# Optimization experiments

Measured on AMD Instinct MI355X. Metric: run time of the kernel, lower is better.

## Reference

```python
import jax, jax.numpy as jnp
import numpy as np

HIDDEN = 1024
HEADS = 16
K = 8
B = 4
S = 2048
LN_EPS = 1e-5


def setup_inputs() -> dict:
    key = jax.random.key(0)
    ks = jax.random.split(key, 16)
    E = HIDDEN
    w = lambda kk, shape: jax.random.normal(kk, shape, dtype=jnp.float32) * 0.02
    return {
        "representations": jax.random.normal(ks[0], (B, S, E), dtype=jnp.float32),
        "attention_mask": jnp.zeros((B, S), dtype=jnp.float32),
        "queries": jax.random.normal(ks[1], (K, E), dtype=jnp.float32),
        "Wq": w(ks[2], (K, E, E)), "bq": jnp.zeros((K, E), jnp.float32),
        "Wk": w(ks[3], (K, E, E)), "bk": jnp.zeros((K, E), jnp.float32),
        "Wv": w(ks[4], (K, E, E)), "bv": jnp.zeros((K, E), jnp.float32),
        "Wo": w(ks[5], (K, E, E)), "bo": jnp.zeros((K, E), jnp.float32),
        "Wp": w(ks[6], (K, E, E)), "bp": jnp.zeros((K, E), jnp.float32),
        "gamma": jnp.ones((E,), jnp.float32),
        "beta": jnp.zeros((E,), jnp.float32),
    }


def reference(representations, attention_mask, queries, Wq, bq, Wk, bk, Wv, bv,
              Wo, bo, Wp, bp, gamma, beta):
    k, E = queries.shape
    Bq, Sq, _ = representations.shape
    H = HEADS
    Dh = E // H
    # per-k query projection (query length is 1)
    q = jnp.einsum('ke,kfe->kf', queries, Wq) + bq          # (k, E)
    q = q.reshape(k, H, Dh) * (Dh ** -0.5)                  # (k, H, Dh)
    # stacked key/value projections across all k attention layers
    Kp = jnp.einsum('bse,kfe->kbsf', representations, Wk) + bk[:, None, None, :]
    Vp = jnp.einsum('bse,kfe->kbsf', representations, Wv) + bv[:, None, None, :]
    Kp = Kp.reshape(k, Bq, Sq, H, Dh)
    Vp = Vp.reshape(k, Bq, Sq, H, Dh)
    # single-query attention scores, additive float mask per batch over keys
    scores = jnp.einsum('khd,kbshd->kbhs', q, Kp)           # (k, B, H, S)
    scores = scores + attention_mask[None, :, None, :]
    probs = jax.nn.softmax(scores, axis=-1)
    ctx = jnp.einsum('kbhs,kbshd->kbhd', probs, Vp).reshape(k, Bq, E)
    # MHA out_proj, then per-k output projection
    attn_out = jnp.einsum('kbe,kfe->kbf', ctx, Wo) + bo[:, None, :]
    out = jnp.einsum('kbe,kfe->kbf', attn_out, Wp) + bp[:, None, :]
    # concat along query-slot dim -> (B, k, E), then LayerNorm over E
    out = out.transpose(1, 0, 2)
    mu = out.mean(-1, keepdims=True)
    var = ((out - mu) ** 2).mean(-1, keepdims=True)
    return gamma * (out - mu) * jax.lax.rsqrt(var + LN_EPS) + beta
```

## Files before the change

### kernel.cpp

```cpp
#include <hip/hip_runtime.h>
#include <hip/hip_bf16.h>
#include <stdint.h>

#define E_  1024
#define H_  16
#define D_  64
#define K_  8
#define B_  4
#define S_  2048
#define KH_ 128

typedef __attribute__((ext_vector_type(8))) short   short8;
typedef __attribute__((ext_vector_type(8))) ushort  ushort8;
typedef __attribute__((ext_vector_type(4))) ushort  ushort4v;
typedef __attribute__((ext_vector_type(4))) float   f32x4;

__device__ __forceinline__ ushort f2bf(float x){
  union { float f; uint32_t u; } v; v.f = x;
  return (ushort)((v.u + 0x7FFFu + ((v.u >> 16) & 1u)) >> 16);
}

__device__ __forceinline__ void lds_barrier(){
  asm volatile("s_waitcnt lgkmcnt(0)" ::: "memory");
  __builtin_amdgcn_s_barrier();
}

__global__ __launch_bounds__(256) void k1_qs(const float* __restrict__ queries,
                                             const float* __restrict__ Wq,
                                             const float* __restrict__ bq,
                                             float* __restrict__ qs){
  int gw = (blockIdx.x * 256 + threadIdx.x) >> 6;
  int lane = threadIdx.x & 63;
  int k = gw >> 10, f = gw & 1023;
  const float* wrow = Wq + ((size_t)(k*E_) + f)*E_;
  const float* qrow = queries + k*E_;
  float acc = 0.f;
  #pragma unroll
  for (int j = 0; j < 4; j++){
    int e = (j*64 + lane)*4;
    float4 w = *(const float4*)(wrow + e);
    float4 q = *(const float4*)(qrow + e);
    acc += w.x*q.x + w.y*q.y + w.z*q.z + w.w*q.w;
  }
  #pragma unroll
  for (int off = 32; off; off >>= 1) acc += __shfl_down(acc, off);
  if (lane == 0) qs[k*E_ + f] = (acc + bq[k*E_ + f]) * 0.125f;
}

__global__ __launch_bounds__(256) void k2_qk(const float* __restrict__ qs,
                                             const float* __restrict__ Wk,
                                             const float* __restrict__ bk,
                                             ushort* __restrict__ qkb,
                                             float* __restrict__ qb){
  int bid = blockIdx.x;
  int eq = bid & 3;
  int kh = bid >> 2;
  int k = kh >> 4, h = kh & 15;
  __shared__ float qsh[64];
  int t = threadIdx.x;
  if (t < 64) qsh[t] = qs[k*E_ + h*64 + t];
  __syncthreads();
  int e = eq*256 + t;
  const float* wbase = Wk + ((size_t)(k*E_) + h*64)*E_ + e;
  float a = 0.f;
  #pragma unroll 8
  for (int d = 0; d < 64; d++) a += qsh[d] * wbase[(size_t)d*E_];
  qkb[kh*E_ + e] = f2bf(a);
  if (eq == 0 && t == 0){
    float s = 0.f;
    for (int d = 0; d < 64; d++) s += qsh[d] * bk[k*E_ + h*64 + d];
    qb[kh] = s;
  }
}

__global__ __launch_bounds__(256) void k3_scores(const float* __restrict__ rep,
                                                 const ushort* __restrict__ qkb,
                                                 float* __restrict__ scoresP){
  __shared__ __align__(16) ushort As[2][64][40];
  __shared__ __align__(16) ushort Bs[2][128][40];
  int bid = blockIdx.x;
  int ks = bid & 3, m = (bid >> 2) & 31, b = bid >> 7;
  int t = threadIdx.x, wv = t >> 6, lane = t & 63;
  int l0 = lane & 15, l1 = lane >> 4;
  int wr = wv >> 1, wc = wv & 1;
  int arow = t >> 2, acg = t & 3;
  int brow = t >> 1, bhalf = t & 1;
  const float*  aSrc = rep + ((size_t)(b*S_) + m*64 + arow)*E_ + ks*256 + acg*4;
  const ushort* bSrc = qkb + (size_t)brow*E_ + ks*256 + bhalf*16;

  f32x4 acc[2][4];
  #pragma unroll
  for (int mt = 0; mt < 2; mt++)
    #pragma unroll
    for (int nt = 0; nt < 4; nt++) acc[mt][nt] = (f32x4){0.f,0.f,0.f,0.f};

  float4  va[2][2];
  ushort8 vb[2][2];
  #pragma unroll
  for (int p = 0; p < 2; p++){
    va[p][0] = *(const float4*)(aSrc + p*32);
    va[p][1] = *(const float4*)(aSrc + p*32 + 16);
    vb[p][0] = *(const ushort8*)(bSrc + p*32);
    vb[p][1] = *(const ushort8*)(bSrc + p*32 + 8);
  }
  #pragma unroll
  for (int j = 0; j < 2; j++){
    ushort4v u;
    u[0]=f2bf(va[0][j].x); u[1]=f2bf(va[0][j].y); u[2]=f2bf(va[0][j].z); u[3]=f2bf(va[0][j].w);
    *(ushort4v*)&As[0][arow][acg*4 + j*16] = u;
    *(ushort8*)&Bs[0][brow][bhalf*16 + j*8] = vb[0][j];
  }
  lds_barrier();

  #pragma unroll
  for (int c = 0; c < 8; c++){
    const int cur = c & 1;
    short8 af[2], bf[4];
    #pragma unroll
    for (int mt = 0; mt < 2; mt++)
      af[mt] = *(const short8*)&As[cur][wr*32 + mt*16 + l0][l1*8];
    #pragma unroll
    for (int nt = 0; nt < 4; nt++)
      bf[nt] = *(const short8*)&Bs[cur][wc*64 + nt*16 + l0][l1*8];
    #pragma unroll
    for (int mt = 0; mt < 2; mt++)
      #pragma unroll
      for (int nt = 0; nt < 4; nt++)
        acc[mt][nt] = __builtin_amdgcn_mfma_f32_16x16x32_bf16(af[mt], bf[nt], acc[mt][nt], 0,0,0);
    if (c < 6){
      const int p = c & 1;
      va[p][0] = *(const float4*)(aSrc + (c+2)*32);
      va[p][1] = *(const float4*)(aSrc + (c+2)*32 + 16);
      vb[p][0] = *(const ushort8*)(bSrc + (c+2)*32);
      vb[p][1] = *(const ushort8*)(bSrc + (c+2)*32 + 8);
    }
    if (c < 7){
      const int p = (c+1) & 1;
      #pragma unroll
      for (int j = 0; j < 2; j++){
        ushort4v u;
        u[0]=f2bf(va[p][j].x); u[1]=f2bf(va[p][j].y); u[2]=f2bf(va[p][j].z); u[3]=f2bf(va[p][j].w);
        *(ushort4v*)&As[p][arow][acg*4 + j*16] = u;
        *(ushort8*)&Bs[p][brow][bhalf*16 + j*8] = vb[p][j];
      }
    }
    lds_barrier();
  }
  float* obase = scoresP + (size_t)ks*((size_t)B_*KH_*S_) + (size_t)(b*KH_)*S_;
  #pragma unroll
  for (int mt = 0; mt < 2; mt++){
    #pragma unroll
    for (int nt = 0; nt < 4; nt++){
      int kh = wc*64 + nt*16 + l0;
      int s  = m*64 + wr*32 + mt*16 + l1*4;
      float* op = obase + (size_t)kh*S_ + s;
      #pragma unroll
      for (int r = 0; r < 4; r++) op[r] = acc[mt][nt][r];
    }
  }
}

__global__ __launch_bounds__(256) void k4_softmax(const float* __restrict__ scoresP,
                                                  const float* __restrict__ qb,
                                                  const float* __restrict__ mask,
                                                  ushort* __restrict__ probs,
                                                  float* __restrict__ wrep){
  __shared__ float red[4];
  const size_t P = (size_t)B_*KH_*S_;
  int row = blockIdx.x;
  int b = row >> 7, kh = row & 127;
  int t = threadIdx.x, wv = t >> 6, lane = t & 63;
  {
    float4 z = {0.f, 0.f, 0.f, 0.f};
    *(float4*)(wrep + ((size_t)blockIdx.x*1024 + t*4)) = z;
  }
  const float* x = scoresP + (size_t)row * S_ + t*8;
  const float* mrow = mask + b*S_ + t*8;
  float qbv = qb[kh];
  float v[8];
  #pragma unroll
  for (int h = 0; h < 2; h++){
    float4 p0 = *(const float4*)(x + h*4);
    float4 p1 = *(const float4*)(x + h*4 + P);
    float4 p2 = *(const float4*)(x + h*4 + 2*P);
    float4 p3 = *(const float4*)(x + h*4 + 3*P);
    float4 mm = *(const float4*)(mrow + h*4);
    v[h*4+0] = (p0.x + p1.x) + (p2.x + p3.x) + qbv + mm.x;
    v[h*4+1] = (p0.y + p1.y) + (p2.y + p3.y) + qbv + mm.y;
    v[h*4+2] = (p0.z + p1.z) + (p2.z + p3.z) + qbv + mm.z;
    v[h*4+3] = (p0.w + p1.w) + (p2.w + p3.w) + qbv + mm.w;
  }
  float m = v[0];
  #pragma unroll
  for (int i = 1; i < 8; i++) m = fmaxf(m, v[i]);
  #pragma unroll
  for (int off = 32; off; off >>= 1) m = fmaxf(m, __shfl_down(m, off));
  if (lane == 0) red[wv] = m;
  __syncthreads();
  float M = fmaxf(fmaxf(red[0], red[1]), fmaxf(red[2], red[3]));
  __syncthreads();
  float s = 0.f;
  #pragma unroll
  for (int i = 0; i < 8; i++){ v[i] = __expf(v[i] - M); s += v[i]; }
  #pragma unroll
  for (int off = 32; off; off >>= 1) s += __shfl_down(s, off);
  if (lane == 0) red[wv] = s;
  __syncthreads();
  float inv = 1.0f / (red[0] + red[1] + red[2] + red[3]);
  ushort8 o;
  #pragma unroll
  for (int i = 0; i < 8; i++) o[i] = f2bf(v[i] * inv);
  *(ushort8*)(probs + (size_t)row*S_ + t*8) = o;
}

__global__ __launch_bounds__(256) void k5_wrep(const ushort* __restrict__ probs,
                                               const float* __restrict__ rep,
                                               float* __restrict__ wrep){
  __shared__ __align__(16) ushort As[2][128][40];
  __shared__ __align__(16) ushort Bs[2][64][40];
  int bid = blockIdx.x;
  int et = bid & 15, b = (bid >> 4) & 3, sp = bid >> 6;
  int t = threadIdx.x, wv = t >> 6, lane = t & 63;
  int l0 = lane & 15, l1 = lane >> 4;
  int wr = wv >> 1, wc = wv & 1;
  int arow = t >> 1, ahalf = t & 1;
  int bsrow = t >> 3, beg = t & 7;
  const ushort* aSrc = probs + (size_t)(b*KH_ + arow)*S_ + sp*256 + ahalf*16;
  const float*  bSrc = rep + ((size_t)(b*S_) + sp*256 + bsrow)*E_ + et*64 + beg*8;

  f32x4 acc[4][2];
  #pragma unroll
  for (int mt = 0; mt < 4; mt++)
    #pragma unroll
    for (int nt = 0; nt < 2; nt++) acc[mt][nt] = (f32x4){0.f,0.f,0.f,0.f};

  ushort8 va[2][2];
  float4  vb[2][2];
  #pragma unroll
  for (int p = 0; p < 2; p++){
    va[p][0] = *(const ushort8*)(aSrc + p*32);
    va[p][1] = *(const ushort8*)(aSrc + p*32 + 8);
    vb[p][0] = *(const float4*)(bSrc + (size_t)(p*32)*E_);
    vb[p][1] = *(const float4*)(bSrc + (size_t)(p*32)*E_ + 4);
  }
  {
    *(ushort8*)&As[0][arow][ahalf*16]     = va[0][0];
    *(ushort8*)&As[0][arow][ahalf*16 + 8] = va[0][1];
    int rot = (beg & 3) * 8;
    int sw = (bsrow + rot) & 31;
    #pragma unroll
    for (int j = 0; j < 2; j++){
      float vv[4] = {vb[0][j].x, vb[0][j].y, vb[0][j].z, vb[0][j].w};
      #pragma unroll
      for (int jj = 0; jj < 4; jj++)
        Bs[0][beg*8 + j*4 + jj][sw] = f2bf(vv[jj]);
    }
  }
  lds_barrier();

  #pragma unroll
  for (int c = 0; c < 8; c++){
    const int cur = c & 1;
    short8 af[4], bf[2];
    #pragma unroll
    for (int mt = 0; mt < 4; mt++)
      af[mt] = *(const short8*)&As[cur][wr*64 + mt*16 + l0][l1*8];
    #pragma unroll
    for (int nt = 0; nt < 2; nt++){
      int e_loc = wc*32 + nt*16 + l0;
      int sstart = (l1*8 + ((e_loc >> 3) & 3)*8) & 31;
      bf[nt] = *(const short8*)&Bs[cur][e_loc][sstart];
    }
    #pragma unroll
    for (int mt = 0; mt < 4; mt++)
      #pragma unroll
      for (int nt = 0; nt < 2; nt++)
        acc[mt][nt] = __builtin_amdgcn_mfma_f32_16x16x32_bf16(af[mt], bf[nt], acc[mt][nt], 0,0,0);
    if (c < 6){
      const int p = c & 1;
      va[p][0] = *(const ushort8*)(aSrc + (c+2)*32);
      va[p][1] = *(const ushort8*)(aSrc + (c+2)*32 + 8);
      vb[p][0] = *(const float4*)(bSrc + (size_t)((c+2)*32)*E_);
      vb[p][1] = *(const float4*)(bSrc + (size_t)((c+2)*32)*E_ + 4);
    }
    if (c < 7){
      const int p = (c+1) & 1;
      *(ushort8*)&As[p][arow][ahalf*16]     = va[p][0];
      *(ushort8*)&As[p][arow][ahalf*16 + 8] = va[p][1];
      int rot = (beg & 3) * 8;
      int sw = (bsrow + rot) & 31;
      #pragma unroll
      for (int j = 0; j < 2; j++){
        float vv[4] = {vb[p][j].x, vb[p][j].y, vb[p][j].z, vb[p][j].w};
        #pragma unroll
        for (int jj = 0; jj < 4; jj++)
          Bs[p][beg*8 + j*4 + jj][sw] = f2bf(vv[jj]);
      }
    }
    lds_barrier();
  }
  float* obase = wrep + (size_t)(b*KH_)*E_ + et*64;
  #pragma unroll
  for (int mt = 0; mt < 4; mt++){
    #pragma unroll
    for (int nt = 0; nt < 2; nt++){
      int kh = wr*64 + mt*16 + l1*4;
      int e  = wc*32 + nt*16 + l0;
      #pragma unroll
      for (int r = 0; r < 4; r++)
        unsafeAtomicAdd(&obase[(size_t)(kh + r)*E_ + e], acc[mt][nt][r]);
    }
  }
}

__global__ __launch_bounds__(256) void k6_ctx(const float* __restrict__ wrep,
                                              const float* __restrict__ Wv,
                                              const float* __restrict__ bv,
                                              float* __restrict__ ctx){
  int gw = (blockIdx.x*256 + threadIdx.x) >> 6;
  int lane = threadIdx.x & 63;
  int k = gw >> 10, f = gw & 1023;
  int h = f >> 6;
  const float* wrow = Wv + ((size_t)(k*E_) + f)*E_;
  const float* x0 = wrep + ((size_t)(0*KH_) + k*16 + h)*E_;
  const float* x1 = wrep + ((size_t)(1*KH_) + k*16 + h)*E_;
  const float* x2 = wrep + ((size_t)(2*KH_) + k*16 + h)*E_;
  const float* x3 = wrep + ((size_t)(3*KH_) + k*16 + h)*E_;
  float a0=0.f, a1=0.f, a2=0.f, a3=0.f;
  #pragma unroll
  for (int j = 0; j < 4; j++){
    int e = (j*64 + lane)*4;
    float4 w = *(const float4*)(wrow + e);
    float4 p;
    p = *(const float4*)(x0+e); a0 += w.x*p.x + w.y*p.y + w.z*p.z + w.w*p.w;
    p = *(const float4*)(x1+e); a1 += w.x*p.x + w.y*p.y + w.z*p.z + w.w*p.w;
    p = *(const float4*)(x2+e); a2 += w.x*p.x + w.y*p.y + w.z*p.z + w.w*p.w;
    p = *(const float4*)(x3+e); a3 += w.x*p.x + w.y*p.y + w.z*p.z + w.w*p.w;
  }
  #pragma unroll
  for (int off = 32; off; off >>= 1){
    a0 += __shfl_down(a0, off); a1 += __shfl_down(a1, off);
    a2 += __shfl_down(a2, off); a3 += __shfl_down(a3, off);
  }
  if (lane == 0){
    float bvv = bv[k*E_ + f];
    ctx[((size_t)(k*B_) + 0)*E_ + f] = a0 + bvv;
    ctx[((size_t)(k*B_) + 1)*E_ + f] = a1 + bvv;
    ctx[((size_t)(k*B_) + 2)*E_ + f] = a2 + bvv;
    ctx[((size_t)(k*B_) + 3)*E_ + f] = a3 + bvv;
  }
}

__global__ __launch_bounds__(256) void gemv_kb(const float* __restrict__ in,
                                               const float* __restrict__ W,
                                               const float* __restrict__ bias,
                                               float* __restrict__ outp){
  int gw = (blockIdx.x*256 + threadIdx.x) >> 6;
  int lane = threadIdx.x & 63;
  int k = gw >> 10, f = gw & 1023;
  const float* wrow = W + ((size_t)(k*E_) + f)*E_;
  const float* x0 = in + ((size_t)(k*B_) + 0)*E_;
  const float* x1 = in + ((size_t)(k*B_) + 1)*E_;
  const float* x2 = in + ((size_t)(k*B_) + 2)*E_;
  const float* x3 = in + ((size_t)(k*B_) + 3)*E_;
  float a0=0.f, a1=0.f, a2=0.f, a3=0.f;
  #pragma unroll
  for (int j = 0; j < 4; j++){
    int e = (j*64 + lane)*4;
    float4 w = *(const float4*)(wrow + e);
    float4 p;
    p = *(const float4*)(x0+e); a0 += w.x*p.x + w.y*p.y + w.z*p.z + w.w*p.w;
    p = *(const float4*)(x1+e); a1 += w.x*p.x + w.y*p.y + w.z*p.z + w.w*p.w;
    p = *(const float4*)(x2+e); a2 += w.x*p.x + w.y*p.y + w.z*p.z + w.w*p.w;
    p = *(const float4*)(x3+e); a3 += w.x*p.x + w.y*p.y + w.z*p.z + w.w*p.w;
  }
  #pragma unroll
  for (int off = 32; off; off >>= 1){
    a0 += __shfl_down(a0, off); a1 += __shfl_down(a1, off);
    a2 += __shfl_down(a2, off); a3 += __shfl_down(a3, off);
  }
  if (lane == 0){
    float bb = bias[k*E_ + f];
    outp[((size_t)(k*B_) + 0)*E_ + f] = a0 + bb;
    outp[((size_t)(k*B_) + 1)*E_ + f] = a1 + bb;
    outp[((size_t)(k*B_) + 2)*E_ + f] = a2 + bb;
    outp[((size_t)(k*B_) + 3)*E_ + f] = a3 + bb;
  }
}

__global__ __launch_bounds__(256) void k9_ln(const float* __restrict__ outkb,
                                             const float* __restrict__ gamma,
                                             const float* __restrict__ beta,
                                             float* __restrict__ out){
  __shared__ float rs[4], rs2[4];
  int row = blockIdx.x;
  int b = row >> 3, k = row & 7;
  int t = threadIdx.x, wv = t >> 6, lane = t & 63;
  const float* x = outkb + ((size_t)(k*B_) + b)*E_;
  float4 v = *(const float4*)(x + t*4);
  float s  = v.x + v.y + v.z + v.w;
  float s2 = v.x*v.x + v.y*v.y + v.z*v.z + v.w*v.w;
  #pragma unroll
  for (int off = 32; off; off >>= 1){ s += __shfl_down(s, off); s2 += __shfl_down(s2, off); }
  if (lane == 0){ rs[wv] = s; rs2[wv] = s2; }
  __syncthreads();
  float S  = rs[0] + rs[1] + rs[2] + rs[3];
  float S2 = rs2[0] + rs2[1] + rs2[2] + rs2[3];
  float mu = S * (1.0f/E_);
  float var = S2 * (1.0f/E_) - mu*mu;
  float inv = rsqrtf(var + 1e-5f);
  float4 g  = *(const float4*)(gamma + t*4);
  float4 bt = *(const float4*)(beta + t*4);
  float4 o;
  o.x = g.x*(v.x-mu)*inv + bt.x;
  o.y = g.y*(v.y-mu)*inv + bt.y;
  o.z = g.z*(v.z-mu)*inv + bt.z;
  o.w = g.w*(v.w-mu)*inv + bt.w;
  *(float4*)(out + ((size_t)(b*K_) + k)*E_ + t*4) = o;
}

extern "C" void kernel_launch(void* const* d_in, const int* in_sizes, int n_in,
                              void* d_out, int out_size, void* d_ws, size_t ws_size,
                              hipStream_t stream){
  const float* rep     = (const float*)d_in[0];
  const float* mask    = (const float*)d_in[1];
  const float* queries = (const float*)d_in[2];
  const float* Wq = (const float*)d_in[3];
  const float* bq = (const float*)d_in[4];
  const float* Wk = (const float*)d_in[5];
  const float* bk = (const float*)d_in[6];
  const float* Wv = (const float*)d_in[7];
  const float* bv = (const float*)d_in[8];
  const float* Wo = (const float*)d_in[9];
  const float* bo = (const float*)d_in[10];
  const float* Wp = (const float*)d_in[11];
  const float* bp = (const float*)d_in[12];
  const float* gamma = (const float*)d_in[13];
  const float* beta  = (const float*)d_in[14];
  float* out = (float*)d_out;

  char* ws = (char*)d_ws;
  size_t off = 0;
  float*  qs     = (float*)(ws + off);  off += (size_t)K_*E_*4;
  ushort* qkb    = (ushort*)(ws + off); off += (size_t)KH_*E_*2;
  float*  qb     = (float*)(ws + off);  off += 1024;
  float*  scoresP= (float*)(ws + off);  off += (size_t)4*B_*KH_*S_*4;
  ushort* probs  = (ushort*)(ws + off); off += (size_t)B_*KH_*S_*2;
  float*  wrep   = (float*)(ws + off);  off += (size_t)B_*KH_*E_*4;
  float*  ctx    = (float*)(ws + off);  off += (size_t)K_*B_*E_*4;
  float*  attn   = (float*)(ws + off);  off += (size_t)K_*B_*E_*4;
  float*  outkb  = (float*)(ws + off);  off += (size_t)K_*B_*E_*4;

  k1_qs     <<<2048, 256, 0, stream>>>(queries, Wq, bq, qs);
  k2_qk     <<<512,  256, 0, stream>>>(qs, Wk, bk, qkb, qb);
  k3_scores <<<512,  256, 0, stream>>>(rep, qkb, scoresP);
  k4_softmax<<<512,  256, 0, stream>>>(scoresP, qb, mask, probs, wrep);
  k5_wrep   <<<512,  256, 0, stream>>>(probs, rep, wrep);
  k6_ctx    <<<2048, 256, 0, stream>>>(wrep, Wv, bv, ctx);
  gemv_kb   <<<2048, 256, 0, stream>>>(ctx, Wo, bo, attn);
  gemv_kb   <<<2048, 256, 0, stream>>>(attn, Wp, bp, outkb);
  k9_ln     <<<32,   256, 0, stream>>>(outkb, gamma, beta, out);
}
```

Baseline: 85.55 us.

## Store split-K partials in bf16 and replace atomics with combine kernel

```diff
diff --git a/kernel.cpp b/kernel.cpp
--- a/kernel.cpp
+++ b/kernel.cpp
@@ -18,6 +18,9 @@
 __device__ __forceinline__ ushort f2bf(float x){
   union { float f; uint32_t u; } v; v.f = x;
   return (ushort)((v.u + 0x7FFFu + ((v.u >> 16) & 1u)) >> 16);
+}
+__device__ __forceinline__ float bf2f(ushort u){
+  union { uint32_t u32; float f; } v; v.u32 = ((uint32_t)u) << 16; return v.f;
 }
 
 __device__ __forceinline__ void lds_barrier(){
@@ -75,7 +78,7 @@
 
 __global__ __launch_bounds__(256) void k3_scores(const float* __restrict__ rep,
                                                  const ushort* __restrict__ qkb,
-                                                 float* __restrict__ scoresP){
+                                                 ushort* __restrict__ scoresPb){
   __shared__ __align__(16) ushort As[2][64][40];
   __shared__ __align__(16) ushort Bs[2][128][40];
   int bid = blockIdx.x;
@@ -146,49 +149,47 @@
     }
     lds_barrier();
   }
-  float* obase = scoresP + (size_t)ks*((size_t)B_*KH_*S_) + (size_t)(b*KH_)*S_;
+  ushort* obase = scoresPb + (size_t)ks*((size_t)B_*KH_*S_) + (size_t)(b*KH_)*S_;
   #pragma unroll
   for (int mt = 0; mt < 2; mt++){
     #pragma unroll
     for (int nt = 0; nt < 4; nt++){
       int kh = wc*64 + nt*16 + l0;
       int s  = m*64 + wr*32 + mt*16 + l1*4;
-      float* op = obase + (size_t)kh*S_ + s;
-      #pragma unroll
-      for (int r = 0; r < 4; r++) op[r] = acc[mt][nt][r];
-    }
-  }
-}
-
-__global__ __launch_bounds__(256) void k4_softmax(const float* __restrict__ scoresP,
+      ushort4v u;
+      u[0] = f2bf(acc[mt][nt][0]);
+      u[1] = f2bf(acc[mt][nt][1]);
+      u[2] = f2bf(acc[mt][nt][2]);
+      u[3] = f2bf(acc[mt][nt][3]);
+      *(ushort4v*)(obase + (size_t)kh*S_ + s) = u;
+    }
+  }
+}
+
+__global__ __launch_bounds__(256) void k4_softmax(const ushort* __restrict__ scoresPb,
                                                   const float* __restrict__ qb,
                                                   const float* __restrict__ mask,
-                                                  ushort* __restrict__ probs,
-                                                  float* __restrict__ wrep){
+                                                  ushort* __restrict__ probs){
   __shared__ float red[4];
   const size_t P = (size_t)B_*KH_*S_;
   int row = blockIdx.x;
   int b = row >> 7, kh = row & 127;
   int t = threadIdx.x, wv = t >> 6, lane = t & 63;
-  {
-    float4 z = {0.f, 0.f, 0.f, 0.f};
-    *(float4*)(wrep + ((size_t)blockIdx.x*1024 + t*4)) = z;
-  }
-  const float* x = scoresP + (size_t)row * S_ + t*8;
+  const ushort* x = scoresPb + (size_t)row * S_ + t*8;
   const float* mrow = mask + b*S_ + t*8;
   float qbv = qb[kh];
-  float v[8];
-  #pragma unroll
-  for (int h = 0; h < 2; h++){
-    float4 p0 = *(const float4*)(x + h*4);
-    float4 p1 = *(const float4*)(x + h*4 + P);
-    float4 p2 = *(const float4*)(x + h*4 + 2*P);
-    float4 p3 = *(const float4*)(x + h*4 + 3*P);
-    float4 mm = *(const float4*)(mrow + h*4);
-    v[h*4+0] = (p0.x + p1.x) + (p2.x + p3.x) + qbv + mm.x;
-    v[h*4+1] = (p0.y + p1.y) + (p2.y + p3.y) + qbv + mm.y;
-    v[h*4+2] = (p0.z + p1.z) + (p2.z + p3.z) + qbv + mm.z;
-    v[h*4+3] = (p0.w + p1.w) + (p2.w + p3.w) + qbv + mm.w;
+  float v[8] = {0.f,0.f,0.f,0.f,0.f,0.f,0.f,0.f};
+  #pragma unroll
+  for (int p = 0; p < 4; p++){
+    ushort8 up = *(const ushort8*)(x + (size_t)p*P);
+    #pragma unroll
+    for (int i = 0; i < 8; i++) v[i] += bf2f(up[i]);
+  }
+  {
+    float4 m0 = *(const float4*)(mrow);
+    float4 m1 = *(const float4*)(mrow + 4);
+    v[0] += qbv + m0.x; v[1] += qbv + m0.y; v[2] += qbv + m0.z; v[3] += qbv + m0.w;
+    v[4] += qbv + m1.x; v[5] += qbv + m1.y; v[6] += qbv + m1.z; v[7] += qbv + m1.w;
   }
   float m = v[0];
   #pragma unroll
@@ -215,7 +216,7 @@
 
 __global__ __launch_bounds__(256) void k5_wrep(const ushort* __restrict__ probs,
                                                const float* __restrict__ rep,
-                                               float* __restrict__ wrep){
+                                               ushort* __restrict__ wrepPb){
   __shared__ __align__(16) ushort As[2][128][40];
   __shared__ __align__(16) ushort Bs[2][64][40];
   int bid = blockIdx.x;
@@ -299,7 +300,7 @@
     }
     lds_barrier();
   }
-  float* obase = wrep + (size_t)(b*KH_)*E_ + et*64;
+  ushort* obase = wrepPb + (size_t)sp*((size_t)B_*KH_*E_) + (size_t)(b*KH_)*E_ + et*64;
   #pragma unroll
   for (int mt = 0; mt < 4; mt++){
     #pragma unroll
@@ -308,9 +309,26 @@
       int e  = wc*32 + nt*16 + l0;
       #pragma unroll
       for (int r = 0; r < 4; r++)
-        unsafeAtomicAdd(&obase[(size_t)(kh + r)*E_ + e], acc[mt][nt][r]);
-    }
-  }
+        obase[(size_t)(kh + r)*E_ + e] = f2bf(acc[mt][nt][r]);
+    }
+  }
+}
+
+__global__ __launch_bounds__(256) void k6c_comb(const ushort* __restrict__ wrepPb,
+                                                float* __restrict__ wrep){
+  const size_t P = (size_t)B_*KH_*E_;
+  size_t i = ((size_t)blockIdx.x * 256 + threadIdx.x) * 8;
+  float a[8] = {0.f,0.f,0.f,0.f,0.f,0.f,0.f,0.f};
+  #pragma unroll
+  for (int p = 0; p < 8; p++){
+    ushort8 u = *(const ushort8*)(wrepPb + i + (size_t)p*P);
+    #pragma unroll
+    for (int j = 0; j < 8; j++) a[j] += bf2f(u[j]);
+  }
+  f32x4 o0 = {a[0], a[1], a[2], a[3]};
+  f32x4 o1 = {a[4], a[5], a[6], a[7]};
+  *(f32x4*)(wrep + i)     = o0;
+  *(f32x4*)(wrep + i + 4) = o1;
 }
 
 __global__ __launch_bounds__(256) void k6_ctx(const float* __restrict__ wrep,
@@ -441,21 +459,23 @@
 
   char* ws = (char*)d_ws;
   size_t off = 0;
-  float*  qs     = (float*)(ws + off);  off += (size_t)K_*E_*4;
-  ushort* qkb    = (ushort*)(ws + off); off += (size_t)KH_*E_*2;
-  float*  qb     = (float*)(ws + off);  off += 1024;
-  float*  scoresP= (float*)(ws + off);  off += (size_t)4*B_*KH_*S_*4;
-  ushort* probs  = (ushort*)(ws + off); off += (size_t)B_*KH_*S_*2;
-  float*  wrep   = (float*)(ws + off);  off += (size_t)B_*KH_*E_*4;
-  float*  ctx    = (float*)(ws + off);  off += (size_t)K_*B_*E_*4;
-  float*  attn   = (float*)(ws + off);  off += (size_t)K_*B_*E_*4;
-  float*  outkb  = (float*)(ws + off);  off += (size_t)K_*B_*E_*4;
+  float*  qs      = (float*)(ws + off);  off += (size_t)K_*E_*4;
+  ushort* qkb     = (ushort*)(ws + off); off += (size_t)KH_*E_*2;
+  float*  qb      = (float*)(ws + off);  off += 1024;
+  ushort* scoresPb= (ushort*)(ws + off); off += (size_t)4*B_*KH_*S_*2;
+  ushort* probs   = (ushort*)(ws + off); off += (size_t)B_*KH_*S_*2;
+  ushort* wrepPb  = (ushort*)(ws + off); off += (size_t)8*B_*KH_*E_*2;
+  float*  wrep    = (float*)(ws + off);  off += (size_t)B_*KH_*E_*4;
+  float*  ctx     = (float*)(ws + off);  off += (size_t)K_*B_*E_*4;
+  float*  attn    = (float*)(ws + off);  off += (size_t)K_*B_*E_*4;
+  float*  outkb   = (float*)(ws + off);  off += (size_t)K_*B_*E_*4;
 
   k1_qs     <<<2048, 256, 0, stream>>>(queries, Wq, bq, qs);
   k2_qk     <<<512,  256, 0, stream>>>(qs, Wk, bk, qkb, qb);
-  k3_scores <<<512,  256, 0, stream>>>(rep, qkb, scoresP);
-  k4_softmax<<<512,  256, 0, stream>>>(scoresP, qb, mask, probs, wrep);
-  k5_wrep   <<<512,  256, 0, stream>>>(probs, rep, wrep);
+  k3_scores <<<512,  256, 0, stream>>>(rep, qkb, scoresPb);
+  k4_softmax<<<512,  256, 0, stream>>>(scoresPb, qb, mask, probs);
+  k5_wrep   <<<512,  256, 0, stream>>>(probs, rep, wrepPb);
+  k6c_comb  <<<256,  256, 0, stream>>>(wrepPb, wrep);
   k6_ctx    <<<2048, 256, 0, stream>>>(wrep, Wv, bv, ctx);
   gemv_kb   <<<2048, 256, 0, stream>>>(ctx, Wo, bo, attn);
   gemv_kb   <<<2048, 256, 0, stream>>>(attn, Wp, bp, outkb);
```

Result: faster. 77.00 us (-10.0%).
